# Performance work log

Measured on AMD Instinct MI355X. Metric: run time of the kernel, lower is better.

The kernel has to match this reference:

```python
import jax, jax.numpy as jnp
import numpy as np

N_NODES = 50000
N_EDGES = 1_600_000
IN_CH = 128
HID = 128


def setup_inputs() -> dict:
    key = jax.random.key(0)
    ks = jax.random.split(key, 8)
    x = jax.random.normal(ks[0], (N_NODES, IN_CH), dtype=jnp.float32)
    edge_index = jax.random.randint(ks[1], (2, N_EDGES), 0, N_NODES, dtype=jnp.int64)
    def glorot(k, shape):
        fan_in, fan_out = shape
        s = jnp.sqrt(6.0 / (fan_in + fan_out))
        return jax.random.uniform(k, shape, jnp.float32, -s, s)
    return {
        "x": x,
        "edge_index": edge_index,
        "W1": glorot(ks[2], (IN_CH, HID)), "b1": jnp.zeros((HID,), jnp.float32),
        "W2": glorot(ks[3], (HID, HID)), "b2": jnp.zeros((HID,), jnp.float32),
        "W_age": glorot(ks[4], (HID, 3)), "b_age": jnp.zeros((3,), jnp.float32),
        "W_sex": glorot(ks[5], (HID, 2)), "b_sex": jnp.zeros((2,), jnp.float32),
        "W_eth": glorot(ks[6], (HID, 3)), "b_eth": jnp.zeros((3,), jnp.float32),
    }


def _prep_graph(edge_index, n_nodes):
    # PyG GCNConv default: add self-loops, symmetric normalization.
    loops = jnp.arange(n_nodes, dtype=edge_index.dtype)
    src = jnp.concatenate([edge_index[0], loops])
    dst = jnp.concatenate([edge_index[1], loops])
    deg = jax.ops.segment_sum(jnp.ones_like(dst, jnp.float32), dst, num_segments=n_nodes)
    dinv = jnp.where(deg > 0, jax.lax.rsqrt(deg), 0.0)
    norm = dinv[src] * dinv[dst]  # [E+N]
    return src, dst, norm


def _gcn_conv(x, W, b, src, dst, norm, n_nodes):
    h = x @ W                              # [N, out] linear transform first
    msg = h[src] * norm[:, None]           # gather + normalize
    out = jax.ops.segment_sum(msg, dst, num_segments=n_nodes)  # scatter-add
    return out + b


def reference(x, edge_index, W1, b1, W2, b2, W_age, b_age, W_sex, b_sex, W_eth, b_eth):
    n = x.shape[0]
    src, dst, norm = _prep_graph(edge_index, n)
    h = jax.nn.relu(_gcn_conv(x, W1, b1, src, dst, norm, n))
    h = jax.nn.relu(_gcn_conv(h, W2, b2, src, dst, norm, n))
    age = _gcn_conv(h, W_age, b_age, src, dst, norm, n)
    sex = _gcn_conv(h, W_sex, b_sex, src, dst, norm, n)
    eth = _gcn_conv(h, W_eth, b_eth, src, dst, norm, n)
    return age, sex, eth
```

## Files before the change

### kernel.cpp

```cpp
#include <hip/hip_runtime.h>
#include <hip/hip_fp16.h>


#define NBUK_MAX 512

typedef float vfloat2 __attribute__((ext_vector_type(2)));

__global__ __launch_bounds__(256) void k_bhist(const int* __restrict__ dst, int E, int nbuk,
                                               int* __restrict__ bcount) {
    __shared__ int h[NBUK_MAX];
    int tid = threadIdx.x;
    for (int i = tid; i < nbuk; i += 256) h[i] = 0;
    __syncthreads();
    int s0 = blockIdx.x * 4096;
#pragma unroll
    for (int i = 0; i < 16; i++) {
        int e = s0 + i * 256 + tid;
        if (e < E) atomicAdd(&h[dst[e] >> 7], 1);
    }
    __syncthreads();
    for (int i = tid; i < nbuk; i += 256)
        if (h[i]) atomicAdd(&bcount[i], h[i]);
}

__global__ __launch_bounds__(512) void k_bscan(const int* __restrict__ bcount, int nb,
                                               int* __restrict__ bbase, int* __restrict__ bcur) {
    __shared__ int s[512];
    int tid = threadIdx.x;
    int v = (tid < nb) ? bcount[tid] : 0;
    s[tid] = v;
    __syncthreads();
    for (int off = 1; off < 512; off <<= 1) {
        int t = (tid >= off) ? s[tid - off] : 0;
        __syncthreads();
        s[tid] += t;
        __syncthreads();
    }
    if (tid < nb) {
        int excl = s[tid] - v;
        bbase[tid] = excl;
        bcur[tid] = excl;
        if (tid == nb - 1) bbase[nb] = s[tid];
    }
}

__global__ __launch_bounds__(256) void k_passA(const int* __restrict__ src,
                                               const int* __restrict__ dst, int E, int nbuk,
                                               int* __restrict__ bcur,
                                               unsigned* __restrict__ bbuf) {
    __shared__ int h[NBUK_MAX];
    __shared__ int base[NBUK_MAX];
    __shared__ int lcur[NBUK_MAX];
    int tid = threadIdx.x;
    for (int i = tid; i < nbuk; i += 256) h[i] = 0;
    __syncthreads();
    int s0 = blockIdx.x * 4096;
#pragma unroll
    for (int i = 0; i < 16; i++) {
        int e = s0 + i * 256 + tid;
        if (e < E) atomicAdd(&h[dst[e] >> 7], 1);
    }
    __syncthreads();
    for (int i = tid; i < nbuk; i += 256) {
        int c = h[i];
        base[i] = c ? atomicAdd(&bcur[i], c) : 0;
        lcur[i] = 0;
    }
    __syncthreads();
#pragma unroll
    for (int i = 0; i < 16; i++) {
        int e = s0 + i * 256 + tid;
        if (e < E) {
            int d = dst[e];
            int b = d >> 7;
            int idx = atomicAdd(&lcur[b], 1);
            bbuf[base[b] + idx] = ((unsigned)d << 16) | (unsigned)src[e];
        }
    }
}

__global__ __launch_bounds__(256) void k_passB(const unsigned* __restrict__ bbuf,
                                               const int* __restrict__ bbase, int N,
                                               int* __restrict__ row_ptr,
                                               float* __restrict__ dinv,
                                               unsigned short* __restrict__ sorted) {
    __shared__ int h[128], sc[128], lc[128];
    int b = blockIdx.x, tid = threadIdx.x;
    int node0 = b << 7;
    int ncnt = min(128, N - node0);
    int s = bbase[b], e = bbase[b + 1];
    if (tid < 128) h[tid] = 0;
    __syncthreads();
    for (int i = s + tid; i < e; i += 256) atomicAdd(&h[(bbuf[i] >> 16) & 127], 1);
    __syncthreads();
    if (tid < 128) sc[tid] = h[tid];
    __syncthreads();
    for (int off = 1; off < 128; off <<= 1) {
        int t = 0;
        if (tid < 128 && tid >= off) t = sc[tid - off];
        __syncthreads();
        if (tid < 128) sc[tid] += t;
        __syncthreads();
    }
    if (tid < ncnt) {
        int excl = sc[tid] - h[tid];
        row_ptr[node0 + tid] = s + excl;
        dinv[node0 + tid] = rsqrtf((float)(h[tid] + 1));
        lc[tid] = excl;
    }
    if (b == gridDim.x - 1 && tid == 0) row_ptr[N] = e;
    __syncthreads();
    for (int i = s + tid; i < e; i += 256) {
        unsigned p = bbuf[i];
        int nl = (p >> 16) & 127;
        int idx = atomicAdd(&lc[nl], 1);
        sorted[s + idx] = (unsigned short)(p & 0xffffu);
    }
}

__global__ __launch_bounds__(256) void k_gemm_scale_h(const float* __restrict__ in,
                                                      const float* __restrict__ W,
                                                      const float* __restrict__ dinv, int N,
                                                      __half* __restrict__ out) {
    __shared__ float Ws[32][128];
    __shared__ float Xs[32][64];
    int tid = threadIdx.x;
    int row0 = blockIdx.x * 64;
    int tc = tid & 15;
    int tr = tid >> 4;
    float acc[4][8];
#pragma unroll
    for (int i = 0; i < 4; i++)
#pragma unroll
        for (int j = 0; j < 8; j++) acc[i][j] = 0.f;

    for (int k0 = 0; k0 < 128; k0 += 32) {
#pragma unroll
        for (int j = 0; j < 4; j++) {
            int u = tid + j * 256;
            int kk = u >> 5, c4 = u & 31;
            *(float4*)&Ws[kk][c4 * 4] = *(const float4*)&W[(k0 + kk) * 128 + c4 * 4];
        }
#pragma unroll
        for (int j = 0; j < 2; j++) {
            int u = tid + j * 256;
            int r = u >> 3, kq = u & 7;
            int row = row0 + r;
            if (row > N - 1) row = N - 1;
            float4 v = *(const float4*)&in[(size_t)row * 128 + k0 + kq * 4];
            Xs[kq * 4 + 0][r] = v.x;
            Xs[kq * 4 + 1][r] = v.y;
            Xs[kq * 4 + 2][r] = v.z;
            Xs[kq * 4 + 3][r] = v.w;
        }
        __syncthreads();
#pragma unroll 8
        for (int kk = 0; kk < 32; kk++) {
            float4 xv = *(const float4*)&Xs[kk][tr * 4];
            float4 wa = *(const float4*)&Ws[kk][tc * 8];
            float4 wb = *(const float4*)&Ws[kk][tc * 8 + 4];
            float xr[4] = {xv.x, xv.y, xv.z, xv.w};
            float wc[8] = {wa.x, wa.y, wa.z, wa.w, wb.x, wb.y, wb.z, wb.w};
#pragma unroll
            for (int i = 0; i < 4; i++)
#pragma unroll
                for (int j = 0; j < 8; j++) acc[i][j] += xr[i] * wc[j];
        }
        __syncthreads();
    }
#pragma unroll
    for (int i = 0; i < 4; i++) {
        int row = row0 + tr * 4 + i;
        if (row < N) {
            float di = dinv[row];
            union {
                uint4 u;
                __half h[8];
            } pk;
#pragma unroll
            for (int j = 0; j < 8; j++) pk.h[j] = __float2half_rn(di * acc[i][j]);
            *(uint4*)&out[(size_t)row * 128 + tc * 8] = pk.u;
        }
    }
}

__global__ __launch_bounds__(256) void k_agg128h(const __half* __restrict__ hs,
                                                 const int* __restrict__ row_ptr,
                                                 const unsigned short* __restrict__ ss,
                                                 const float* __restrict__ dinv,
                                                 const float* __restrict__ bias, int N,
                                                 int do_relu, float* __restrict__ out) {
    int wid = threadIdx.x >> 6;
    int lane = threadIdx.x & 63;
    int node = blockIdx.x * 4 + wid;
    if (node >= N) return;
    const __half2* hp = (const __half2*)hs;
    float2 acc = __half22float2(hp[(size_t)node * 64 + lane]);
    int s = row_ptr[node], e = row_ptr[node + 1];
    int i = s;
    for (; i + 8 <= e; i += 8) {
        int id[8];
#pragma unroll
        for (int u = 0; u < 8; u++) id[u] = __builtin_nontemporal_load(&ss[i + u]);
        float2 v[8];
#pragma unroll
        for (int u = 0; u < 8; u++) v[u] = __half22float2(hp[(size_t)id[u] * 64 + lane]);
        float sx0 = (v[0].x + v[1].x) + (v[2].x + v[3].x);
        float sx1 = (v[4].x + v[5].x) + (v[6].x + v[7].x);
        float sy0 = (v[0].y + v[1].y) + (v[2].y + v[3].y);
        float sy1 = (v[4].y + v[5].y) + (v[6].y + v[7].y);
        acc.x += sx0 + sx1;
        acc.y += sy0 + sy1;
    }
    for (; i < e; i++) {
        float2 v0 = __half22float2(hp[(size_t)ss[i] * 64 + lane]);
        acc.x += v0.x;
        acc.y += v0.y;
    }
    float di = dinv[node];
    int c = lane * 2;
    float2 b = *(const float2*)&bias[c];
    float ox = di * acc.x + b.x;
    float oy = di * acc.y + b.y;
    if (do_relu) {
        ox = fmaxf(ox, 0.f);
        oy = fmaxf(oy, 0.f);
    }
    vfloat2 o;
    o.x = ox;
    o.y = oy;
    __builtin_nontemporal_store(o, (vfloat2*)&out[(size_t)node * 128 + c]);
}

__global__ __launch_bounds__(256) void k_headgemm(const float* __restrict__ h,
                                                  const float* __restrict__ Wa,
                                                  const float* __restrict__ Wsx,
                                                  const float* __restrict__ We,
                                                  const float* __restrict__ dinv, int N,
                                                  float* __restrict__ ths) {
    __shared__ float Ws8[128][8];
    int tid = threadIdx.x;
#pragma unroll
    for (int j = 0; j < 4; j++) {
        int u = tid + j * 256;
        int k = u >> 3, c = u & 7;
        float v;
        if (c < 3) v = Wa[k * 3 + c];
        else if (c < 5) v = Wsx[k * 2 + (c - 3)];
        else v = We[k * 3 + (c - 5)];
        Ws8[k][c] = v;
    }
    __syncthreads();
    int node = blockIdx.x * 32 + (tid >> 3);
    int col = tid & 7;
    if (node >= N) return;
    const float* hr = &h[(size_t)node * 128];
    float acc = 0.f;
#pragma unroll 4
    for (int k = 0; k < 128; k += 4) {
        float4 hv = *(const float4*)&hr[k];
        acc += hv.x * Ws8[k][col] + hv.y * Ws8[k + 1][col] + hv.z * Ws8[k + 2][col] +
               hv.w * Ws8[k + 3][col];
    }
    ths[(size_t)node * 8 + col] = dinv[node] * acc;
}

__global__ __launch_bounds__(256) void k_agg8(const float* __restrict__ ths,
                                              const int* __restrict__ row_ptr,
                                              const unsigned short* __restrict__ ss,
                                              const float* __restrict__ dinv,
                                              const float* __restrict__ ba,
                                              const float* __restrict__ bs,
                                              const float* __restrict__ be, int N,
                                              float* __restrict__ outp) {
    int tid = threadIdx.x;
    int node = blockIdx.x * 32 + (tid >> 3);
    int j = tid & 7;
    if (node >= N) return;
    float acc = ths[(size_t)node * 8 + j];
    int s = row_ptr[node], e = row_ptr[node + 1];
    for (int i = s; i < e; i++) {
        int sc = ss[i];
        acc += ths[(size_t)sc * 8 + j];
    }
    float bias = (j < 3) ? ba[j] : ((j < 5) ? bs[j - 3] : be[j - 5]);
    float v = dinv[node] * acc + bias;
    if (j < 3) outp[(size_t)node * 3 + j] = v;
    else if (j < 5) outp[(size_t)N * 3 + (size_t)node * 2 + (j - 3)] = v;
    else outp[(size_t)N * 5 + (size_t)node * 3 + (j - 5)] = v;
}

extern "C" void kernel_launch(void* const* d_in, const int* in_sizes, int n_in,
                              void* d_out, int out_size, void* d_ws, size_t ws_size,
                              hipStream_t stream) {
    const float* x = (const float*)d_in[0];
    const int* edge = (const int*)d_in[1];
    const float* W1 = (const float*)d_in[2];
    const float* b1 = (const float*)d_in[3];
    const float* W2 = (const float*)d_in[4];
    const float* b2 = (const float*)d_in[5];
    const float* Wa = (const float*)d_in[6];
    const float* ba = (const float*)d_in[7];
    const float* Wsx = (const float*)d_in[8];
    const float* bs = (const float*)d_in[9];
    const float* We = (const float*)d_in[10];
    const float* be = (const float*)d_in[11];

    int N = in_sizes[0] / 128;
    int E = in_sizes[1] / 2;
    const int* srcp = edge;
    const int* dstp = edge + E;
    int nbuk = (N + 127) >> 7;

    char* ws = (char*)d_ws;
    size_t off = 0;
    auto alloc = [&](size_t bytes) -> char* {
        char* p = ws + off;
        off += (bytes + 255) & ~(size_t)255;
        return p;
    };
    int* bcount = (int*)alloc((size_t)(nbuk + 1) * 4);
    int* bbase = (int*)alloc((size_t)(nbuk + 1) * 4);
    int* bcur = (int*)alloc((size_t)(nbuk + 1) * 4);
    int* row_ptr = (int*)alloc((size_t)(N + 1) * 4);
    float* dinv = (float*)alloc((size_t)N * 4);
    unsigned* bbuf = (unsigned*)alloc((size_t)E * 4);
    unsigned short* sorted = (unsigned short*)alloc((size_t)E * 2);
    __half* bufH = (__half*)alloc((size_t)N * 128 * 2);
    float* bufF = (float*)alloc((size_t)N * 128 * 4);
    float* ths = (float*)alloc((size_t)N * 8 * 4);

    int nbT = (E + 4095) / 4096;

    hipMemsetAsync(bcount, 0, (size_t)(nbuk + 1) * 4, stream);
    k_bhist<<<nbT, 256, 0, stream>>>(dstp, E, nbuk, bcount);
    k_bscan<<<1, 512, 0, stream>>>(bcount, nbuk, bbase, bcur);
    k_passA<<<nbT, 256, 0, stream>>>(srcp, dstp, E, nbuk, bcur, bbuf);
    k_passB<<<nbuk, 256, 0, stream>>>(bbuf, bbase, N, row_ptr, dinv, sorted);

    int gb = (N + 63) / 64;
    k_gemm_scale_h<<<gb, 256, 0, stream>>>(x, W1, dinv, N, bufH);
    k_agg128h<<<(N + 3) / 4, 256, 0, stream>>>(bufH, row_ptr, sorted, dinv, b1, N, 1, bufF);
    k_gemm_scale_h<<<gb, 256, 0, stream>>>(bufF, W2, dinv, N, bufH);
    k_agg128h<<<(N + 3) / 4, 256, 0, stream>>>(bufH, row_ptr, sorted, dinv, b2, N, 1, bufF);
    k_headgemm<<<(N + 31) / 32, 256, 0, stream>>>(bufF, Wa, Wsx, We, dinv, N, ths);
    k_agg8<<<(N + 31) / 32, 256, 0, stream>>>(ths, row_ptr, sorted, dinv, ba, bs, be, N,
                                              (float*)d_out);
}
```

Before: 279.0 us.

## Split fp16 feature table into two 64-channel slices for aggregation

```diff
diff --git a/kernel.cpp b/kernel.cpp
--- a/kernel.cpp
+++ b/kernel.cpp
@@ -3,8 +3,6 @@
 
 
 #define NBUK_MAX 512
-
-typedef float vfloat2 __attribute__((ext_vector_type(2)));
 
 __global__ __launch_bounds__(256) void k_bhist(const int* __restrict__ dst, int E, int nbuk,
                                                int* __restrict__ bcount) {
@@ -179,32 +177,36 @@
             } pk;
 #pragma unroll
             for (int j = 0; j < 8; j++) pk.h[j] = __float2half_rn(di * acc[i][j]);
-            *(uint4*)&out[(size_t)row * 128 + tc * 8] = pk.u;
-        }
-    }
-}
-
-__global__ __launch_bounds__(256) void k_agg128h(const __half* __restrict__ hs,
-                                                 const int* __restrict__ row_ptr,
-                                                 const unsigned short* __restrict__ ss,
-                                                 const float* __restrict__ dinv,
-                                                 const float* __restrict__ bias, int N,
-                                                 int do_relu, float* __restrict__ out) {
+            *(uint4*)&out[((size_t)(tc >> 3) * N + row) * 64 + (tc & 7) * 8] = pk.u;
+        }
+    }
+}
+
+__global__ __launch_bounds__(256) void k_agg64s(const __half* __restrict__ hs,
+                                                const int* __restrict__ row_ptr,
+                                                const unsigned short* __restrict__ ss,
+                                                const float* __restrict__ dinv,
+                                                const float* __restrict__ bias, int N,
+                                                int do_relu, float* __restrict__ out) {
+    int slice = blockIdx.x & 1;
+    int nb = blockIdx.x >> 1;
     int wid = threadIdx.x >> 6;
     int lane = threadIdx.x & 63;
-    int node = blockIdx.x * 4 + wid;
+    int node = nb * 4 + wid;
     if (node >= N) return;
-    const __half2* hp = (const __half2*)hs;
-    float2 acc = __half22float2(hp[(size_t)node * 64 + lane]);
+    int g = lane >> 5;
+    int c = lane & 31;
+    const __half2* hp = (const __half2*)(hs + (size_t)slice * N * 64);
+    float2 acc = {0.f, 0.f};
     int s = row_ptr[node], e = row_ptr[node + 1];
-    int i = s;
-    for (; i + 8 <= e; i += 8) {
+    int i = s + g;
+    for (; i + 14 < e; i += 16) {
         int id[8];
 #pragma unroll
-        for (int u = 0; u < 8; u++) id[u] = __builtin_nontemporal_load(&ss[i + u]);
+        for (int u = 0; u < 8; u++) id[u] = ss[i + u * 2];
         float2 v[8];
 #pragma unroll
-        for (int u = 0; u < 8; u++) v[u] = __half22float2(hp[(size_t)id[u] * 64 + lane]);
+        for (int u = 0; u < 8; u++) v[u] = __half22float2(hp[(size_t)id[u] * 32 + c]);
         float sx0 = (v[0].x + v[1].x) + (v[2].x + v[3].x);
         float sx1 = (v[4].x + v[5].x) + (v[6].x + v[7].x);
         float sy0 = (v[0].y + v[1].y) + (v[2].y + v[3].y);
@@ -212,24 +214,27 @@
         acc.x += sx0 + sx1;
         acc.y += sy0 + sy1;
     }
-    for (; i < e; i++) {
-        float2 v0 = __half22float2(hp[(size_t)ss[i] * 64 + lane]);
+    for (; i < e; i += 2) {
+        float2 v0 = __half22float2(hp[(size_t)ss[i] * 32 + c]);
         acc.x += v0.x;
         acc.y += v0.y;
     }
-    float di = dinv[node];
-    int c = lane * 2;
-    float2 b = *(const float2*)&bias[c];
-    float ox = di * acc.x + b.x;
-    float oy = di * acc.y + b.y;
-    if (do_relu) {
-        ox = fmaxf(ox, 0.f);
-        oy = fmaxf(oy, 0.f);
-    }
-    vfloat2 o;
-    o.x = ox;
-    o.y = oy;
-    __builtin_nontemporal_store(o, (vfloat2*)&out[(size_t)node * 128 + c]);
+    acc.x += __shfl_xor(acc.x, 32);
+    acc.y += __shfl_xor(acc.y, 32);
+    if (g == 0) {
+        float2 sv = __half22float2(hp[(size_t)node * 32 + c]);
+        acc.x += sv.x;
+        acc.y += sv.y;
+        float di = dinv[node];
+        float2 b = *(const float2*)&bias[slice * 64 + c * 2];
+        float ox = di * acc.x + b.x;
+        float oy = di * acc.y + b.y;
+        if (do_relu) {
+            ox = fmaxf(ox, 0.f);
+            oy = fmaxf(oy, 0.f);
+        }
+        *(float2*)&out[(size_t)node * 128 + slice * 64 + c * 2] = {ox, oy};
+    }
 }
 
 __global__ __launch_bounds__(256) void k_headgemm(const float* __restrict__ h,
@@ -339,10 +344,11 @@
     k_passB<<<nbuk, 256, 0, stream>>>(bbuf, bbase, N, row_ptr, dinv, sorted);
 
     int gb = (N + 63) / 64;
+    int agrid = 2 * ((N + 3) / 4);
     k_gemm_scale_h<<<gb, 256, 0, stream>>>(x, W1, dinv, N, bufH);
-    k_agg128h<<<(N + 3) / 4, 256, 0, stream>>>(bufH, row_ptr, sorted, dinv, b1, N, 1, bufF);
+    k_agg64s<<<agrid, 256, 0, stream>>>(bufH, row_ptr, sorted, dinv, b1, N, 1, bufF);
     k_gemm_scale_h<<<gb, 256, 0, stream>>>(bufF, W2, dinv, N, bufH);
-    k_agg128h<<<(N + 3) / 4, 256, 0, stream>>>(bufH, row_ptr, sorted, dinv, b2, N, 1, bufF);
+    k_agg64s<<<agrid, 256, 0, stream>>>(bufH, row_ptr, sorted, dinv, b2, N, 1, bufF);
     k_headgemm<<<(N + 31) / 32, 256, 0, stream>>>(bufF, Wa, Wsx, We, dinv, N, ths);
     k_agg8<<<(N + 31) / 32, 256, 0, stream>>>(ths, row_ptr, sorted, dinv, ba, bs, be, N,
                                               (float*)d_out);
```

Result: slower. 295.2 us (+5.8%).
